# Optimization experiments

Measured on AMD Instinct MI355X. Metric: run time of the kernel, lower is better.

The kernel has to match this reference:

```python
import jax, jax.numpy as jnp
import numpy as np

B, N, DIM, DD = 8, 4096, 512, 512
SCALE = DD ** -0.5


def setup_inputs() -> dict:
    key = jax.random.key(0)
    ks = jax.random.split(key, 8)
    x = jax.random.normal(ks[0], (B, N, DIM), dtype=jnp.float32)
    mask = jnp.ones((B, N), dtype=bool)
    # torch nn.Linear(dim, decode_dim, bias=False): weight [DD, DIM], y = x @ W.T
    Wq = jax.random.normal(ks[1], (DD, DIM), dtype=jnp.float32) * (DIM ** -0.5)
    Wk = jax.random.normal(ks[2], (DD, DIM), dtype=jnp.float32) * (DIM ** -0.5)
    Wv = jax.random.normal(ks[3], (DD, DIM), dtype=jnp.float32) * (DIM ** -0.5)
    Wr = jax.random.normal(ks[4], (DD, DD), dtype=jnp.float32) * (DD ** -0.5)
    w_alpha = jax.random.normal(ks[5], (DD,), dtype=jnp.float32)
    w_beta = jax.random.normal(ks[6], (DD,), dtype=jnp.float32)
    return {"x": x, "Wq": Wq, "Wk": Wk, "Wv": Wv, "Wr": Wr,
            "w_alpha": w_alpha, "w_beta": w_beta, "mask": mask}


def _masked_softmax_n(logits, mask):
    # softmax over axis=1 (N), with -inf where mask is False
    logits = jnp.where(mask[:, :, None], logits, -jnp.inf)
    return jax.nn.softmax(logits, axis=1)


def reference(x, Wq, Wk, Wv, Wr, w_alpha, w_beta, mask):
    q = jnp.einsum('bnf,df->bnd', x, Wq)          # [B,N,DD]
    k = jnp.einsum('bnf,df->bnd', x, Wk)
    v = jnp.einsum('bnf,df->bnd', x, Wv)
    alpha = _masked_softmax_n(q * w_alpha * SCALE, mask)   # [B,N,DD]
    global_query = jnp.einsum('bnd,bnd->bd', q, alpha)     # [B,DD]
    p = global_query[:, None, :] * k                       # [B,N,DD]
    beta = _masked_softmax_n(p * w_beta * SCALE, mask)
    global_key = jnp.einsum('bnd,bnd->bd', p, beta)        # [B,DD]
    kv = global_key[:, None, :] * v                        # [B,N,DD]
    out = jnp.einsum('bnd,ed->bne', kv, Wr) + q
    return out
```

## Files before the change

kernel.cpp:

```cpp
#include <hip/hip_runtime.h>

#define N_    4096
#define DD_   512
#define SCALE_ 0.044194173824159216f

typedef unsigned short u16;
typedef __attribute__((ext_vector_type(8))) short bf16x8;
typedef __attribute__((ext_vector_type(4))) float f32x4;

__device__ __forceinline__ float bf2f(u16 u) {
    union { unsigned i; float f; } c; c.i = ((unsigned)u) << 16; return c.f;
}
__device__ __forceinline__ u16 f2bf(float f) {
    union { float f; unsigned u; } c; c.f = f;
    unsigned r = c.u + 0x7FFFu + ((c.u >> 16) & 1u);
    return (u16)(r >> 16);
}
__device__ __forceinline__ void gl_lds(const u16* g, u16* l) {
    __builtin_amdgcn_global_load_lds(
        (const __attribute__((address_space(1))) void*)g,
        (__attribute__((address_space(3))) void*)l, 16, 0, 0);
}

__global__ void cvt_x(const float* __restrict__ s, u16* __restrict__ d)
{
    const size_t i = ((size_t)blockIdx.x * 256 + threadIdx.x) * 8;
    float4 f0 = *(const float4*)(s + i), f1 = *(const float4*)(s + i + 4);
    u16 o[8];
    o[0]=f2bf(f0.x); o[1]=f2bf(f0.y); o[2]=f2bf(f0.z); o[3]=f2bf(f0.w);
    o[4]=f2bf(f1.x); o[5]=f2bf(f1.y); o[6]=f2bf(f1.z); o[7]=f2bf(f1.w);
    *(uint4*)(d + i) = *(uint4*)o;
}

__global__ void cvt_w(const float* s0, const float* s1, u16* d0, u16* d1)
{
    const float* s = blockIdx.z ? s1 : s0;
    u16* d = blockIdx.z ? d1 : d0;
    const size_t i = ((size_t)blockIdx.x * 256 + threadIdx.x) * 8;
    float4 f0 = *(const float4*)(s + i), f1 = *(const float4*)(s + i + 4);
    u16 o[8];
    o[0]=f2bf(f0.x); o[1]=f2bf(f0.y); o[2]=f2bf(f0.z); o[3]=f2bf(f0.w);
    o[4]=f2bf(f1.x); o[5]=f2bf(f1.y); o[6]=f2bf(f1.z); o[7]=f2bf(f1.w);
    *(uint4*)(d + i) = *(uint4*)o;
}

__global__ __launch_bounds__(512, 2)
void gemm_red(const u16* __restrict__ A, const u16* __restrict__ Bt,
              const float* __restrict__ coefV, int mode,
              float* T1, float* T2)
{
    const int g = blockIdx.x;
    const int gs = (g & 7) * 32 + (g >> 3);
    const int tileM = gs >> 1;
    const int tileN = gs & 1;
    const int b = tileM >> 4;

    __shared__ __align__(16) char smem[98304];
    float (*rs1)[256] = (float(*)[256])smem;
    float (*rs2)[256] = (float(*)[256])(smem + 8192);

    const int tid = threadIdx.x, wave = tid >> 6, lane = tid & 63;
    const int waveM = wave >> 2, waveN = wave & 3;
    const int l15 = lane & 15, quad = lane >> 4;
    const int l4r = lane >> 2, l4c = lane & 3;

    float cf[4];
    #pragma unroll
    for (int ni = 0; ni < 4; ++ni) {
        const int lcol = waveN * 64 + ni * 16 + l15;
        cf[ni] = mode ? coefV[b * 512 + tileN * 256 + lcol]
                      : coefV[tileN * 256 + lcol] * SCALE_;
    }

    const u16* aPtr = A  + (size_t)(tileM * 256 + wave * 32 + l4r) * 512 + l4c * 8;
    const u16* bPtr = Bt + (size_t)(tileN * 256 + wave * 32 + l4r) * 512 + l4c * 8;

    f32x4 acc[8][4] = {};

    auto STAGE = [&](int k0, int bi) {
        u16* Asb = (u16*)(smem + bi * 32768);
        u16* Bsb = Asb + 8192;
        gl_lds(aPtr + k0,        Asb + wave * 1024);
        gl_lds(aPtr + k0 + 8192, Asb + wave * 1024 + 512);
        gl_lds(bPtr + k0,        Bsb + wave * 1024);
        gl_lds(bPtr + k0 + 8192, Bsb + wave * 1024 + 512);
    };
    auto COMPUTE = [&](int bi) {
        const u16* Ac = (const u16*)(smem + bi * 32768);
        const u16* Bc = Ac + 8192;
        bf16x8 af[8], bfr[4];
        #pragma unroll
        for (int mi = 0; mi < 8; ++mi)
            af[mi] = *(const bf16x8*)&Ac[(waveM * 128 + mi * 16 + l15) * 32 + quad * 8];
        #pragma unroll
        for (int ni = 0; ni < 4; ++ni)
            bfr[ni] = *(const bf16x8*)&Bc[(waveN * 64 + ni * 16 + l15) * 32 + quad * 8];
        #pragma unroll
        for (int mi = 0; mi < 8; ++mi)
            #pragma unroll
            for (int ni = 0; ni < 4; ++ni)
                acc[mi][ni] = __builtin_amdgcn_mfma_f32_16x16x32_bf16(
                    af[mi], bfr[ni], acc[mi][ni], 0, 0, 0);
    };

    STAGE(0, 0);
    STAGE(32, 1);
    asm volatile("s_waitcnt vmcnt(4)" ::: "memory");
    __builtin_amdgcn_s_barrier();

    int bi = 0;
    for (int t = 0; t < 14; ++t) {
        int bs = bi + 2; if (bs >= 3) bs -= 3;
        STAGE((t + 2) * 32, bs);
        COMPUTE(bi);
        asm volatile("s_waitcnt vmcnt(4)" ::: "memory");
        __builtin_amdgcn_s_barrier();
        ++bi; if (bi >= 3) bi = 0;
    }
    COMPUTE(bi);
    asm volatile("s_waitcnt vmcnt(0)" ::: "memory");
    __builtin_amdgcn_s_barrier();
    ++bi; if (bi >= 3) bi = 0;
    COMPUTE(bi);
    __syncthreads();

    float s1[4] = {0.f, 0.f, 0.f, 0.f}, s2[4] = {0.f, 0.f, 0.f, 0.f};
    #pragma unroll
    for (int ni = 0; ni < 4; ++ni)
        #pragma unroll
        for (int mi = 0; mi < 8; ++mi)
            #pragma unroll
            for (int r = 0; r < 4; ++r) {
                float v = acc[mi][ni][r];
                float e = __expf(v * cf[ni]);
                s1[ni] += e; s2[ni] += v * e;
            }

    const int ridx = waveM * 4 + quad;
    #pragma unroll
    for (int ni = 0; ni < 4; ++ni) {
        const int lcol = waveN * 64 + ni * 16 + l15;
        rs1[ridx][lcol] = s1[ni]; rs2[ridx][lcol] = s2[ni];
    }
    __syncthreads();
    if (tid < 256) {
        float a1 = 0.f, a2 = 0.f;
        #pragma unroll
        for (int j = 0; j < 8; ++j) { a1 += rs1[j][tid]; a2 += rs2[j][tid]; }
        atomicAdd(&T1[b * 512 + tileN * 256 + tid], a1);
        atomicAdd(&T2[b * 512 + tileN * 256 + tid], a2);
    }
}

__global__ void comb1_k(const float* __restrict__ T1, const float* __restrict__ T2,
                        const float* __restrict__ wb, float* gq, float* coefK)
{
    const int i = blockIdx.x * 256 + threadIdx.x;
    const float g = T2[i] / T1[i];
    gq[i] = g;
    coefK[i] = g * wb[i & 511] * SCALE_;
}

__global__ void comb2_k(const float* __restrict__ T1, const float* __restrict__ T2,
                        const float* __restrict__ gq, float* gk)
{
    const int i = blockIdx.x * 256 + threadIdx.x;
    gk[i] = gq[i] * (T2[i] / T1[i]);
}

__global__ void transp_cvt(const float* __restrict__ Wv, u16* WvT)
{
    __shared__ float t[32][33];
    const int f0 = (blockIdx.x & 15) * 32, d0 = (blockIdx.x >> 4) * 32;
    const int c = threadIdx.x & 31, r0 = threadIdx.x >> 5;
    #pragma unroll
    for (int p = 0; p < 4; ++p)
        t[r0 + p * 8][c] = Wv[(size_t)(d0 + r0 + p * 8) * 512 + f0 + c];
    __syncthreads();
    #pragma unroll
    for (int p = 0; p < 4; ++p)
        WvT[(size_t)(f0 + r0 + p * 8) * 512 + d0 + c] = f2bf(t[c][r0 + p * 8]);
}

__global__ void scaleA(const float* __restrict__ Wr, const float* __restrict__ gk, u16* Ap)
{
    const size_t idx0 = ((size_t)blockIdx.x * 256 + threadIdx.x) * 8;
    const int b = (int)(idx0 >> 18);
    const int d = (int)(idx0 & 511);
    const size_t ed = idx0 & ((1u << 18) - 1);
    const float* g = gk + b * 512 + d;
    float4 a0 = *(const float4*)(Wr + ed), a1 = *(const float4*)(Wr + ed + 4);
    u16 o[8];
    o[0]=f2bf(a0.x*g[0]); o[1]=f2bf(a0.y*g[1]); o[2]=f2bf(a0.z*g[2]); o[3]=f2bf(a0.w*g[3]);
    o[4]=f2bf(a1.x*g[4]); o[5]=f2bf(a1.y*g[5]); o[6]=f2bf(a1.z*g[6]); o[7]=f2bf(a1.w*g[7]);
    *(uint4*)(Ap + idx0) = *(uint4*)o;
}

__global__ __launch_bounds__(256)
void gemm_w2(const u16* __restrict__ Ap, const u16* __restrict__ Bt,
             u16* __restrict__ C, const float* __restrict__ addF)
{
    const u16* A = Ap + (size_t)blockIdx.z * 262144;
    u16* Cb = C + (size_t)blockIdx.z * 262144;

    __shared__ __align__(16) char smem[32768];
    u16* As0 = (u16*)smem;
    u16* Bs0 = (u16*)(smem + 8192);
    u16* As1 = (u16*)(smem + 16384);
    u16* Bs1 = (u16*)(smem + 24576);

    const int tid = threadIdx.x, wave = tid >> 6, lane = tid & 63;
    const int waveM = wave >> 1, waveN = wave & 1;
    const int l15 = lane & 15, quad = lane >> 4;
    const int l4r = lane >> 2, l4c = lane & 3;
    const int tileN = blockIdx.x, tileM = blockIdx.y;

    f32x4 acc[4][4] = {};
    const u16* aPtr = A  + (size_t)(tileM * 128 + wave * 32 + l4r) * 512 + l4c * 8;
    const u16* bPtr = Bt + (size_t)(tileN * 128 + wave * 32 + l4r) * 512 + l4c * 8;

    auto STAGE = [&](int k0, u16* Asb, u16* Bsb) {
        gl_lds(aPtr + k0,        Asb + wave * 1024);
        gl_lds(aPtr + k0 + 8192, Asb + wave * 1024 + 512);
        gl_lds(bPtr + k0,        Bsb + wave * 1024);
        gl_lds(bPtr + k0 + 8192, Bsb + wave * 1024 + 512);
    };
    auto COMPUTE = [&](const u16* Ac, const u16* Bc) {
        bf16x8 af[4], bfr[4];
        #pragma unroll
        for (int mi = 0; mi < 4; ++mi)
            af[mi] = *(const bf16x8*)&Ac[(waveM * 64 + mi * 16 + l15) * 32 + quad * 8];
        #pragma unroll
        for (int ni = 0; ni < 4; ++ni)
            bfr[ni] = *(const bf16x8*)&Bc[(waveN * 64 + ni * 16 + l15) * 32 + quad * 8];
        #pragma unroll
        for (int mi = 0; mi < 4; ++mi)
            #pragma unroll
            for (int ni = 0; ni < 4; ++ni)
                acc[mi][ni] = __builtin_amdgcn_mfma_f32_16x16x32_bf16(
                    af[mi], bfr[ni], acc[mi][ni], 0, 0, 0);
    };

    STAGE(0, As0, Bs0);
    __syncthreads();
    for (int k0 = 0; k0 < 512; k0 += 64) {
        STAGE(k0 + 32, As1, Bs1);
        COMPUTE(As0, Bs0);
        __syncthreads();
        if (k0 + 64 < 512) STAGE(k0 + 64, As0, Bs0);
        COMPUTE(As1, Bs1);
        __syncthreads();
    }

    #pragma unroll
    for (int mi = 0; mi < 4; ++mi)
        #pragma unroll
        for (int ni = 0; ni < 4; ++ni) {
            const int row = tileM * 128 + waveM * 64 + mi * 16 + quad * 4;
            const int col = tileN * 128 + waveN * 64 + ni * 16 + l15;
            #pragma unroll
            for (int r = 0; r < 4; ++r) {
                float vv = acc[mi][ni][r] + addF[(size_t)(row + r) * 512 + col];
                Cb[(size_t)(row + r) * 512 + col] = f2bf(vv);
            }
        }
}

__global__ __launch_bounds__(512, 2)
void gemm_out(const u16* __restrict__ A, const u16* __restrict__ W2,
              float* __restrict__ out)
{
    const int g = blockIdx.x;
    const int gs = (g & 7) * 32 + (g >> 3);
    const int tileM = gs >> 1, tileN = gs & 1;
    const u16* Bt = W2 + (size_t)(tileM >> 4) * 262144;

    __shared__ __align__(16) char smem[98304];
    float* eb = (float*)smem;

    const int tid = threadIdx.x, wave = tid >> 6, lane = tid & 63;
    const int waveM = wave >> 2, waveN = wave & 3;
    const int l15 = lane & 15, quad = lane >> 4;
    const int l4r = lane >> 2, l4c = lane & 3;

    const u16* aPtr = A  + (size_t)(tileM * 256 + wave * 32 + l4r) * 512 + l4c * 8;
    const u16* bPtr = Bt + (size_t)(tileN * 256 + wave * 32 + l4r) * 512 + l4c * 8;

    f32x4 acc[8][4] = {};

    auto STAGE = [&](int k0, int bi) {
        u16* Asb = (u16*)(smem + bi * 32768);
        u16* Bsb = Asb + 8192;
        gl_lds(aPtr + k0,        Asb + wave * 1024);
        gl_lds(aPtr + k0 + 8192, Asb + wave * 1024 + 512);
        gl_lds(bPtr + k0,        Bsb + wave * 1024);
        gl_lds(bPtr + k0 + 8192, Bsb + wave * 1024 + 512);
    };
    auto COMPUTE = [&](int bi) {
        const u16* Ac = (const u16*)(smem + bi * 32768);
        const u16* Bc = Ac + 8192;
        bf16x8 af[8], bfr[4];
        #pragma unroll
        for (int mi = 0; mi < 8; ++mi)
            af[mi] = *(const bf16x8*)&Ac[(waveM * 128 + mi * 16 + l15) * 32 + quad * 8];
        #pragma unroll
        for (int ni = 0; ni < 4; ++ni)
            bfr[ni] = *(const bf16x8*)&Bc[(waveN * 64 + ni * 16 + l15) * 32 + quad * 8];
        #pragma unroll
        for (int mi = 0; mi < 8; ++mi)
            #pragma unroll
            for (int ni = 0; ni < 4; ++ni)
                acc[mi][ni] = __builtin_amdgcn_mfma_f32_16x16x32_bf16(
                    af[mi], bfr[ni], acc[mi][ni], 0, 0, 0);
    };

    STAGE(0, 0);
    STAGE(32, 1);
    asm volatile("s_waitcnt vmcnt(4)" ::: "memory");
    __builtin_amdgcn_s_barrier();

    int bi = 0;
    for (int t = 0; t < 14; ++t) {
        int bs = bi + 2; if (bs >= 3) bs -= 3;
        STAGE((t + 2) * 32, bs);
        COMPUTE(bi);
        asm volatile("s_waitcnt vmcnt(4)" ::: "memory");
        __builtin_amdgcn_s_barrier();
        ++bi; if (bi >= 3) bi = 0;
    }
    COMPUTE(bi);
    asm volatile("s_waitcnt vmcnt(0)" ::: "memory");
    __builtin_amdgcn_s_barrier();
    ++bi; if (bi >= 3) bi = 0;
    COMPUTE(bi);

    #pragma unroll
    for (int mi = 0; mi < 8; ++mi) {
        __syncthreads();
        #pragma unroll
        for (int ni = 0; ni < 4; ++ni) {
            const int srow = waveM * 16 + quad * 4;
            const int lcol = waveN * 64 + ni * 16 + l15;
            #pragma unroll
            for (int r = 0; r < 4; ++r)
                eb[(srow + r) * 260 + lcol] = acc[mi][ni][r];
        }
        __syncthreads();
        #pragma unroll
        for (int p = 0; p < 4; ++p) {
            const int lr = p * 8 + (tid >> 6);
            const int cp = (tid & 63) * 4;
            const int grow = tileM * 256 + (lr >> 4) * 128 + mi * 16 + (lr & 15);
            float4 vv = *(const float4*)&eb[lr * 260 + cp];
            *(float4*)&out[(size_t)grow * 512 + tileN * 256 + cp] = vv;
        }
    }
}

extern "C" void kernel_launch(void* const* d_in, const int* in_sizes, int n_in,
                              void* d_out, int out_size, void* d_ws, size_t ws_size,
                              hipStream_t stream)
{
    const float* x  = (const float*)d_in[0];
    const float* Wq = (const float*)d_in[1];
    const float* Wk = (const float*)d_in[2];
    const float* Wv = (const float*)d_in[3];
    const float* Wr = (const float*)d_in[4];
    const float* wa = (const float*)d_in[5];
    const float* wb = (const float*)d_in[6];
    float* out = (float*)d_out;

    char* ws = (char*)d_ws;
    float* TQ1   = (float*)(ws);
    float* TQ2   = (float*)(ws + 16 * 1024);
    float* TK1   = (float*)(ws + 32 * 1024);
    float* TK2   = (float*)(ws + 48 * 1024);
    float* gq    = (float*)(ws + 64 * 1024);
    float* coefK = (float*)(ws + 80 * 1024);
    float* gk    = (float*)(ws + 96 * 1024);
    u16*   WvT   = (u16*)  (ws + 112 * 1024);
    u16*   Wqb   = (u16*)  (ws + 624 * 1024);
    u16*   Wkb   = (u16*)  (ws + 1136 * 1024);
    u16*   Ap    = (u16*)  (ws + 1648 * 1024);
    u16*   W2    = (u16*)  (ws + 5744 * 1024);
    u16*   xb    = (u16*)  (ws + 9840 * 1024);

    hipMemsetAsync(TQ1, 0, 64 * 1024, stream);
    cvt_x<<<8192, 256, 0, stream>>>(x, xb);
    cvt_w<<<dim3(128, 1, 2), 256, 0, stream>>>(Wq, Wk, Wqb, Wkb);
    transp_cvt<<<256, 256, 0, stream>>>(Wv, WvT);

    gemm_red<<<256, 512, 0, stream>>>(xb, Wqb, wa, 0, TQ1, TQ2);
    comb1_k<<<16, 256, 0, stream>>>(TQ1, TQ2, wb, gq, coefK);
    gemm_red<<<256, 512, 0, stream>>>(xb, Wkb, coefK, 1, TK1, TK2);
    comb2_k<<<16, 256, 0, stream>>>(TK1, TK2, gq, gk);

    scaleA<<<1024, 256, 0, stream>>>(Wr, gk, Ap);
    gemm_w2<<<dim3(4, 4, 8), 256, 0, stream>>>(Ap, WvT, W2, Wq);

    gemm_out<<<256, 512, 0, stream>>>(xb, W2, out);
}
```

Measured before the change: 216.3 us.

## Split each K-step into two phases with interleaved loads, barriers and MFMA priority

Both GEMM kernels replace the monolithic stage-then-compute step with a two-half K-step. Each half issues part of the LDS fragment reads and half of the next tile's global-to-LDS loads, then syncs and runs an MFMA cluster under raised wave priority (s_setprio). The goal is to interleave memory issue with matrix math across waves, in the style of ping-pong scheduling. It adds extra barriers per K-step, which may cost more than the overlap gains.

```diff
diff --git a/kernel.cpp b/kernel.cpp
--- a/kernel.cpp
+++ b/kernel.cpp
@@ -77,7 +77,57 @@
 
     f32x4 acc[8][4] = {};
 
-    auto STAGE = [&](int k0, int bi) {
+    auto KSTEP = [&](int bi, int bs, int kstage, int vmN) {
+        const u16* Ac = (const u16*)(smem + bi * 32768);
+        const u16* Bc = Ac + 8192;
+        bf16x8 af[8], bfr[4];
+        #pragma unroll
+        for (int mi = 0; mi < 4; ++mi)
+            af[mi] = *(const bf16x8*)&Ac[(waveM * 128 + mi * 16 + l15) * 32 + quad * 8];
+        #pragma unroll
+        for (int ni = 0; ni < 4; ++ni)
+            bfr[ni] = *(const bf16x8*)&Bc[(waveN * 64 + ni * 16 + l15) * 32 + quad * 8];
+        if (kstage >= 0) {
+            u16* Asb = (u16*)(smem + bs * 32768);
+            gl_lds(aPtr + kstage,        Asb + wave * 1024);
+            gl_lds(aPtr + kstage + 8192, Asb + wave * 1024 + 512);
+        }
+        __builtin_amdgcn_s_barrier();
+        asm volatile("s_waitcnt lgkmcnt(0)" ::: "memory");
+        __builtin_amdgcn_sched_barrier(0);
+        __builtin_amdgcn_s_setprio(1);
+        #pragma unroll
+        for (int mi = 0; mi < 4; ++mi)
+            #pragma unroll
+            for (int ni = 0; ni < 4; ++ni)
+                acc[mi][ni] = __builtin_amdgcn_mfma_f32_16x16x32_bf16(
+                    af[mi], bfr[ni], acc[mi][ni], 0, 0, 0);
+        __builtin_amdgcn_s_setprio(0);
+        __builtin_amdgcn_s_barrier();
+        #pragma unroll
+        for (int mi = 4; mi < 8; ++mi)
+            af[mi] = *(const bf16x8*)&Ac[(waveM * 128 + mi * 16 + l15) * 32 + quad * 8];
+        if (kstage >= 0) {
+            u16* Bsb = (u16*)(smem + bs * 32768) + 8192;
+            gl_lds(bPtr + kstage,        Bsb + wave * 1024);
+            gl_lds(bPtr + kstage + 8192, Bsb + wave * 1024 + 512);
+        }
+        __builtin_amdgcn_s_barrier();
+        asm volatile("s_waitcnt lgkmcnt(0)" ::: "memory");
+        __builtin_amdgcn_sched_barrier(0);
+        __builtin_amdgcn_s_setprio(1);
+        #pragma unroll
+        for (int mi = 4; mi < 8; ++mi)
+            #pragma unroll
+            for (int ni = 0; ni < 4; ++ni)
+                acc[mi][ni] = __builtin_amdgcn_mfma_f32_16x16x32_bf16(
+                    af[mi], bfr[ni], acc[mi][ni], 0, 0, 0);
+        __builtin_amdgcn_s_setprio(0);
+        if (vmN == 4)      asm volatile("s_waitcnt vmcnt(4)" ::: "memory");
+        else if (vmN == 0) asm volatile("s_waitcnt vmcnt(0)" ::: "memory");
+        __builtin_amdgcn_s_barrier();
+    };
+    auto STAGE_FULL = [&](int k0, int bi) {
         u16* Asb = (u16*)(smem + bi * 32768);
         u16* Bsb = Asb + 8192;
         gl_lds(aPtr + k0,        Asb + wave * 1024);
@@ -85,43 +135,21 @@
         gl_lds(bPtr + k0,        Bsb + wave * 1024);
         gl_lds(bPtr + k0 + 8192, Bsb + wave * 1024 + 512);
     };
-    auto COMPUTE = [&](int bi) {
-        const u16* Ac = (const u16*)(smem + bi * 32768);
-        const u16* Bc = Ac + 8192;
-        bf16x8 af[8], bfr[4];
-        #pragma unroll
-        for (int mi = 0; mi < 8; ++mi)
-            af[mi] = *(const bf16x8*)&Ac[(waveM * 128 + mi * 16 + l15) * 32 + quad * 8];
-        #pragma unroll
-        for (int ni = 0; ni < 4; ++ni)
-            bfr[ni] = *(const bf16x8*)&Bc[(waveN * 64 + ni * 16 + l15) * 32 + quad * 8];
-        #pragma unroll
-        for (int mi = 0; mi < 8; ++mi)
-            #pragma unroll
-            for (int ni = 0; ni < 4; ++ni)
-                acc[mi][ni] = __builtin_amdgcn_mfma_f32_16x16x32_bf16(
-                    af[mi], bfr[ni], acc[mi][ni], 0, 0, 0);
-    };
-
-    STAGE(0, 0);
-    STAGE(32, 1);
+
+    STAGE_FULL(0, 0);
+    STAGE_FULL(32, 1);
     asm volatile("s_waitcnt vmcnt(4)" ::: "memory");
     __builtin_amdgcn_s_barrier();
 
     int bi = 0;
     for (int t = 0; t < 14; ++t) {
         int bs = bi + 2; if (bs >= 3) bs -= 3;
-        STAGE((t + 2) * 32, bs);
-        COMPUTE(bi);
-        asm volatile("s_waitcnt vmcnt(4)" ::: "memory");
-        __builtin_amdgcn_s_barrier();
+        KSTEP(bi, bs, (t + 2) * 32, 4);
         ++bi; if (bi >= 3) bi = 0;
     }
-    COMPUTE(bi);
-    asm volatile("s_waitcnt vmcnt(0)" ::: "memory");
-    __builtin_amdgcn_s_barrier();
+    KSTEP(bi, 0, -1, 0);
     ++bi; if (bi >= 3) bi = 0;
-    COMPUTE(bi);
+    KSTEP(bi, 0, -1, -1);
     __syncthreads();
 
     float s1[4] = {0.f, 0.f, 0.f, 0.f}, s2[4] = {0.f, 0.f, 0.f, 0.f};
@@ -288,7 +316,57 @@
 
     f32x4 acc[8][4] = {};
 
-    auto STAGE = [&](int k0, int bi) {
+    auto KSTEP = [&](int bi, int bs, int kstage, int vmN) {
+        const u16* Ac = (const u16*)(smem + bi * 32768);
+        const u16* Bc = Ac + 8192;
+        bf16x8 af[8], bfr[4];
+        #pragma unroll
+        for (int mi = 0; mi < 4; ++mi)
+            af[mi] = *(const bf16x8*)&Ac[(waveM * 128 + mi * 16 + l15) * 32 + quad * 8];
+        #pragma unroll
+        for (int ni = 0; ni < 4; ++ni)
+            bfr[ni] = *(const bf16x8*)&Bc[(waveN * 64 + ni * 16 + l15) * 32 + quad * 8];
+        if (kstage >= 0) {
+            u16* Asb = (u16*)(smem + bs * 32768);
+            gl_lds(aPtr + kstage,        Asb + wave * 1024);
+            gl_lds(aPtr + kstage + 8192, Asb + wave * 1024 + 512);
+        }
+        __builtin_amdgcn_s_barrier();
+        asm volatile("s_waitcnt lgkmcnt(0)" ::: "memory");
+        __builtin_amdgcn_sched_barrier(0);
+        __builtin_amdgcn_s_setprio(1);
+        #pragma unroll
+        for (int mi = 0; mi < 4; ++mi)
+            #pragma unroll
+            for (int ni = 0; ni < 4; ++ni)
+                acc[mi][ni] = __builtin_amdgcn_mfma_f32_16x16x32_bf16(
+                    af[mi], bfr[ni], acc[mi][ni], 0, 0, 0);
+        __builtin_amdgcn_s_setprio(0);
+        __builtin_amdgcn_s_barrier();
+        #pragma unroll
+        for (int mi = 4; mi < 8; ++mi)
+            af[mi] = *(const bf16x8*)&Ac[(waveM * 128 + mi * 16 + l15) * 32 + quad * 8];
+        if (kstage >= 0) {
+            u16* Bsb = (u16*)(smem + bs * 32768) + 8192;
+            gl_lds(bPtr + kstage,        Bsb + wave * 1024);
+            gl_lds(bPtr + kstage + 8192, Bsb + wave * 1024 + 512);
+        }
+        __builtin_amdgcn_s_barrier();
+        asm volatile("s_waitcnt lgkmcnt(0)" ::: "memory");
+        __builtin_amdgcn_sched_barrier(0);
+        __builtin_amdgcn_s_setprio(1);
+        #pragma unroll
+        for (int mi = 4; mi < 8; ++mi)
+            #pragma unroll
+            for (int ni = 0; ni < 4; ++ni)
+                acc[mi][ni] = __builtin_amdgcn_mfma_f32_16x16x32_bf16(
+                    af[mi], bfr[ni], acc[mi][ni], 0, 0, 0);
+        __builtin_amdgcn_s_setprio(0);
+        if (vmN == 4)      asm volatile("s_waitcnt vmcnt(4)" ::: "memory");
+        else if (vmN == 0) asm volatile("s_waitcnt vmcnt(0)" ::: "memory");
+        __builtin_amdgcn_s_barrier();
+    };
+    auto STAGE_FULL = [&](int k0, int bi) {
         u16* Asb = (u16*)(smem + bi * 32768);
         u16* Bsb = Asb + 8192;
         gl_lds(aPtr + k0,        Asb + wave * 1024);
@@ -296,43 +374,21 @@
         gl_lds(bPtr + k0,        Bsb + wave * 1024);
         gl_lds(bPtr + k0 + 8192, Bsb + wave * 1024 + 512);
     };
-    auto COMPUTE = [&](int bi) {
-        const u16* Ac = (const u16*)(smem + bi * 32768);
-        const u16* Bc = Ac + 8192;
-        bf16x8 af[8], bfr[4];
-        #pragma unroll
-        for (int mi = 0; mi < 8; ++mi)
-            af[mi] = *(const bf16x8*)&Ac[(waveM * 128 + mi * 16 + l15) * 32 + quad * 8];
-        #pragma unroll
-        for (int ni = 0; ni < 4; ++ni)
-            bfr[ni] = *(const bf16x8*)&Bc[(waveN * 64 + ni * 16 + l15) * 32 + quad * 8];
-        #pragma unroll
-        for (int mi = 0; mi < 8; ++mi)
-            #pragma unroll
-            for (int ni = 0; ni < 4; ++ni)
-                acc[mi][ni] = __builtin_amdgcn_mfma_f32_16x16x32_bf16(
-                    af[mi], bfr[ni], acc[mi][ni], 0, 0, 0);
-    };
-
-    STAGE(0, 0);
-    STAGE(32, 1);
+
+    STAGE_FULL(0, 0);
+    STAGE_FULL(32, 1);
     asm volatile("s_waitcnt vmcnt(4)" ::: "memory");
     __builtin_amdgcn_s_barrier();
 
     int bi = 0;
     for (int t = 0; t < 14; ++t) {
         int bs = bi + 2; if (bs >= 3) bs -= 3;
-        STAGE((t + 2) * 32, bs);
-        COMPUTE(bi);
-        asm volatile("s_waitcnt vmcnt(4)" ::: "memory");
-        __builtin_amdgcn_s_barrier();
+        KSTEP(bi, bs, (t + 2) * 32, 4);
         ++bi; if (bi >= 3) bi = 0;
     }
-    COMPUTE(bi);
-    asm volatile("s_waitcnt vmcnt(0)" ::: "memory");
-    __builtin_amdgcn_s_barrier();
+    KSTEP(bi, 0, -1, 0);
     ++bi; if (bi >= 3) bi = 0;
-    COMPUTE(bi);
+    KSTEP(bi, 0, -1, -1);
 
     #pragma unroll
     for (int mi = 0; mi < 8; ++mi) {
```

Result: no change. 218.3 us (+0.9%).

## Fuse fp32-to-bf16 conversion of x into the first Q GEMM-reduction kernel

Applied to the files above, without the earlier changes.

Removes the standalone cvt_x kernel. The Q GEMM now loads x as fp32 into registers, converts it to bf16, and writes it to LDS. Blocks with tileN==0 also write the bf16 copy to global memory for later GEMMs. This saves one full read of x (64 MB of fp32) and a kernel launch, but the A operand no longer uses async global-to-LDS loads, so register pressure rises and the software pipeline changes.

```diff
diff --git a/kernel.cpp b/kernel.cpp
--- a/kernel.cpp
+++ b/kernel.cpp
@@ -20,16 +20,6 @@
     __builtin_amdgcn_global_load_lds(
         (const __attribute__((address_space(1))) void*)g,
         (__attribute__((address_space(3))) void*)l, 16, 0, 0);
-}
-
-__global__ void cvt_x(const float* __restrict__ s, u16* __restrict__ d)
-{
-    const size_t i = ((size_t)blockIdx.x * 256 + threadIdx.x) * 8;
-    float4 f0 = *(const float4*)(s + i), f1 = *(const float4*)(s + i + 4);
-    u16 o[8];
-    o[0]=f2bf(f0.x); o[1]=f2bf(f0.y); o[2]=f2bf(f0.z); o[3]=f2bf(f0.w);
-    o[4]=f2bf(f1.x); o[5]=f2bf(f1.y); o[6]=f2bf(f1.z); o[7]=f2bf(f1.w);
-    *(uint4*)(d + i) = *(uint4*)o;
 }
 
 __global__ void cvt_w(const float* s0, const float* s1, u16* d0, u16* d1)
@@ -44,10 +34,10 @@
     *(uint4*)(d + i) = *(uint4*)o;
 }
 
-__global__ __launch_bounds__(512, 2)
-void gemm_red(const u16* __restrict__ A, const u16* __restrict__ Bt,
-              const float* __restrict__ coefV, int mode,
-              float* T1, float* T2)
+__global__ __launch_bounds__(512)
+void gemm_redQ(const float* __restrict__ X, const u16* __restrict__ Bt,
+               const float* __restrict__ wa,
+               float* T1, float* T2, u16* __restrict__ xb)
 {
     const int g = blockIdx.x;
     const int gs = (g & 7) * 32 + (g >> 3);
@@ -55,7 +45,7 @@
     const int tileN = gs & 1;
     const int b = tileM >> 4;
 
-    __shared__ __align__(16) char smem[98304];
+    __shared__ __align__(16) char smem[65536];
     float (*rs1)[256] = (float(*)[256])smem;
     float (*rs2)[256] = (float(*)[256])(smem + 8192);
 
@@ -68,8 +58,124 @@
     #pragma unroll
     for (int ni = 0; ni < 4; ++ni) {
         const int lcol = waveN * 64 + ni * 16 + l15;
-        cf[ni] = mode ? coefV[b * 512 + tileN * 256 + lcol]
-                      : coefV[tileN * 256 + lcol] * SCALE_;
+        cf[ni] = wa[tileN * 256 + lcol] * SCALE_;
+    }
+
+    const int aRow = tileM * 256 + wave * 32 + l4r;
+    const float* aF = X  + (size_t)aRow * 512 + l4c * 8;
+    u16* xbp       = xb + (size_t)aRow * 512 + l4c * 8;
+    const u16* bPtr = Bt + (size_t)(tileN * 256 + wave * 32 + l4r) * 512 + l4c * 8;
+
+    f32x4 acc[8][4] = {};
+    float4 pa0, pa1, pa2, pa3;
+
+    auto LOADA = [&](int k0) {
+        pa0 = *(const float4*)(aF + k0);
+        pa1 = *(const float4*)(aF + k0 + 4);
+        pa2 = *(const float4*)(aF + k0 + 8192);
+        pa3 = *(const float4*)(aF + k0 + 8192 + 4);
+    };
+    auto GLDSB = [&](int k0, int bsel) {
+        u16* Bsb = (u16*)(smem + bsel * 32768) + 8192;
+        gl_lds(bPtr + k0,        Bsb + wave * 1024);
+        gl_lds(bPtr + k0 + 8192, Bsb + wave * 1024 + 512);
+    };
+    auto WRITEA = [&](int k0, int bsel) {
+        u16 o[16];
+        o[0]=f2bf(pa0.x);  o[1]=f2bf(pa0.y);  o[2]=f2bf(pa0.z);  o[3]=f2bf(pa0.w);
+        o[4]=f2bf(pa1.x);  o[5]=f2bf(pa1.y);  o[6]=f2bf(pa1.z);  o[7]=f2bf(pa1.w);
+        o[8]=f2bf(pa2.x);  o[9]=f2bf(pa2.y);  o[10]=f2bf(pa2.z); o[11]=f2bf(pa2.w);
+        o[12]=f2bf(pa3.x); o[13]=f2bf(pa3.y); o[14]=f2bf(pa3.z); o[15]=f2bf(pa3.w);
+        u16* Asb = (u16*)(smem + bsel * 32768);
+        *(uint4*)(Asb + wave * 1024 + lane * 8)       = *(uint4*)o;
+        *(uint4*)(Asb + wave * 1024 + 512 + lane * 8) = *(uint4*)(o + 8);
+        if (tileN == 0) {
+            *(uint4*)(xbp + k0)        = *(uint4*)o;
+            *(uint4*)(xbp + k0 + 8192) = *(uint4*)(o + 8);
+        }
+    };
+    auto COMPUTE = [&](int bsel) {
+        const u16* Ac = (const u16*)(smem + bsel * 32768);
+        const u16* Bc = Ac + 8192;
+        bf16x8 af[8], bfr[4];
+        #pragma unroll
+        for (int mi = 0; mi < 8; ++mi)
+            af[mi] = *(const bf16x8*)&Ac[(waveM * 128 + mi * 16 + l15) * 32 + quad * 8];
+        #pragma unroll
+        for (int ni = 0; ni < 4; ++ni)
+            bfr[ni] = *(const bf16x8*)&Bc[(waveN * 64 + ni * 16 + l15) * 32 + quad * 8];
+        #pragma unroll
+        for (int mi = 0; mi < 8; ++mi)
+            #pragma unroll
+            for (int ni = 0; ni < 4; ++ni)
+                acc[mi][ni] = __builtin_amdgcn_mfma_f32_16x16x32_bf16(
+                    af[mi], bfr[ni], acc[mi][ni], 0, 0, 0);
+    };
+
+    LOADA(0); GLDSB(0, 0); WRITEA(0, 0);
+    __syncthreads();
+    int cur = 0;
+    for (int t = 0; t < 16; ++t) {
+        if (t < 15) { LOADA((t + 1) * 32); GLDSB((t + 1) * 32, cur ^ 1); }
+        COMPUTE(cur);
+        if (t < 15) WRITEA((t + 1) * 32, cur ^ 1);
+        __syncthreads();
+        cur ^= 1;
+    }
+
+    float s1[4] = {0.f, 0.f, 0.f, 0.f}, s2[4] = {0.f, 0.f, 0.f, 0.f};
+    #pragma unroll
+    for (int ni = 0; ni < 4; ++ni)
+        #pragma unroll
+        for (int mi = 0; mi < 8; ++mi)
+            #pragma unroll
+            for (int r = 0; r < 4; ++r) {
+                float v = acc[mi][ni][r];
+                float e = __expf(v * cf[ni]);
+                s1[ni] += e; s2[ni] += v * e;
+            }
+
+    const int ridx = waveM * 4 + quad;
+    #pragma unroll
+    for (int ni = 0; ni < 4; ++ni) {
+        const int lcol = waveN * 64 + ni * 16 + l15;
+        rs1[ridx][lcol] = s1[ni]; rs2[ridx][lcol] = s2[ni];
+    }
+    __syncthreads();
+    if (tid < 256) {
+        float a1 = 0.f, a2 = 0.f;
+        #pragma unroll
+        for (int j = 0; j < 8; ++j) { a1 += rs1[j][tid]; a2 += rs2[j][tid]; }
+        atomicAdd(&T1[b * 512 + tileN * 256 + tid], a1);
+        atomicAdd(&T2[b * 512 + tileN * 256 + tid], a2);
+    }
+}
+
+__global__ __launch_bounds__(512, 2)
+void gemm_red(const u16* __restrict__ A, const u16* __restrict__ Bt,
+              const float* __restrict__ coefV,
+              float* T1, float* T2)
+{
+    const int g = blockIdx.x;
+    const int gs = (g & 7) * 32 + (g >> 3);
+    const int tileM = gs >> 1;
+    const int tileN = gs & 1;
+    const int b = tileM >> 4;
+
+    __shared__ __align__(16) char smem[98304];
+    float (*rs1)[256] = (float(*)[256])smem;
+    float (*rs2)[256] = (float(*)[256])(smem + 8192);
+
+    const int tid = threadIdx.x, wave = tid >> 6, lane = tid & 63;
+    const int waveM = wave >> 2, waveN = wave & 3;
+    const int l15 = lane & 15, quad = lane >> 4;
+    const int l4r = lane >> 2, l4c = lane & 3;
+
+    float cf[4];
+    #pragma unroll
+    for (int ni = 0; ni < 4; ++ni) {
+        const int lcol = waveN * 64 + ni * 16 + l15;
+        cf[ni] = coefV[b * 512 + tileN * 256 + lcol];
     }
 
     const u16* aPtr = A  + (size_t)(tileM * 256 + wave * 32 + l4r) * 512 + l4c * 8;
@@ -386,13 +492,12 @@
     u16*   xb    = (u16*)  (ws + 9840 * 1024);
 
     hipMemsetAsync(TQ1, 0, 64 * 1024, stream);
-    cvt_x<<<8192, 256, 0, stream>>>(x, xb);
     cvt_w<<<dim3(128, 1, 2), 256, 0, stream>>>(Wq, Wk, Wqb, Wkb);
     transp_cvt<<<256, 256, 0, stream>>>(Wv, WvT);
 
-    gemm_red<<<256, 512, 0, stream>>>(xb, Wqb, wa, 0, TQ1, TQ2);
+    gemm_redQ<<<256, 512, 0, stream>>>(x, Wqb, wa, TQ1, TQ2, xb);
     comb1_k<<<16, 256, 0, stream>>>(TQ1, TQ2, wb, gq, coefK);
-    gemm_red<<<256, 512, 0, stream>>>(xb, Wkb, coefK, 1, TK1, TK2);
+    gemm_red<<<256, 512, 0, stream>>>(xb, Wkb, coefK, TK1, TK2);
     comb2_k<<<16, 256, 0, stream>>>(TK1, TK2, gq, gk);
 
     scaleA<<<1024, 256, 0, stream>>>(Wr, gk, Ap);
```

Measured after the change: 221.0 us. 2.2% more time.
